# Kernel tuning notes

Hardware: AMD Instinct MI355X
Metric: run time of the kernel (lower is better)

The kernel has to match this reference:

```python
import jax, jax.numpy as jnp
import numpy as np

N = 16384      # points
C = 512        # channels (d_model)
D_INNER = 1024 # expand=2
D_STATE = 16
D_CONV = 4
DT_RANK = 32   # ceil(C/16)
MLP = 1024     # mlp_ratio=2
EPS = 1e-5


def setup_inputs() -> dict:
    key = jax.random.key(0)
    ks = jax.random.split(key, 16)
    s = 0.02
    feat = jax.random.normal(ks[0], (N, C), jnp.float32)
    perm = np.random.RandomState(0).permutation(N)
    order = jnp.asarray(perm, jnp.int32)
    inverse = jnp.asarray(np.argsort(perm), jnp.int32)
    inp = dict(
        feat=feat, order=order, inverse=inverse,
        ln1_w=jnp.ones((C,)), ln1_b=jnp.zeros((C,)),
        in_proj_w=s * jax.random.normal(ks[1], (2 * D_INNER, C)),
        conv_w=s * jax.random.normal(ks[2], (D_INNER, D_CONV)),
        conv_b=jnp.zeros((D_INNER,)),
        x_proj_w=s * jax.random.normal(ks[3], (DT_RANK + 2 * D_STATE, D_INNER)),
        dt_proj_w=s * jax.random.normal(ks[4], (D_INNER, DT_RANK)),
        dt_proj_b=jnp.full((D_INNER,), -2.0),  # softplus(-2) ~ small dt, like mamba init
        A_log=jnp.log(jnp.tile(jnp.arange(1, D_STATE + 1, dtype=jnp.float32)[None, :], (D_INNER, 1))),
        D_skip=jnp.ones((D_INNER,)),
        out_proj_w=s * jax.random.normal(ks[5], (C, D_INNER)),
        ln2_w=jnp.ones((C,)), ln2_b=jnp.zeros((C,)),
        ffn_w1=s * jax.random.normal(ks[6], (C, MLP)), ffn_b1=jnp.zeros((MLP,)),
        ffn_w2=s * jax.random.normal(ks[7], (MLP, C)), ffn_b2=jnp.zeros((C,)),
    )
    return inp


def _layer_norm(x, w, b):
    mu = jnp.mean(x, axis=-1, keepdims=True)
    var = jnp.mean(jnp.square(x - mu), axis=-1, keepdims=True)
    return (x - mu) * jax.lax.rsqrt(var + EPS) * w + b


def _mamba(x, in_proj_w, conv_w, conv_b, x_proj_w, dt_proj_w, dt_proj_b,
           A_log, D_skip, out_proj_w):
    # x: (L, C)
    L = x.shape[0]
    xz = x @ in_proj_w.T                      # (L, 2*D_INNER)
    xm, z = jnp.split(xz, 2, axis=-1)
    # depthwise causal conv1d, kernel D_CONV
    xp = jnp.pad(xm, ((D_CONV - 1, 0), (0, 0)))
    xc = conv_b + sum(xp[k:k + L] * conv_w[:, k] for k in range(D_CONV))
    xc = jax.nn.silu(xc)                      # (L, D_INNER)
    dbc = xc @ x_proj_w.T                     # (L, DT_RANK + 2*D_STATE)
    dt, Bm, Cm = jnp.split(dbc, [DT_RANK, DT_RANK + D_STATE], axis=-1)
    dt = jax.nn.softplus(dt @ dt_proj_w.T + dt_proj_b)  # (L, D_INNER)
    A = -jnp.exp(A_log)                       # (D_INNER, D_STATE)

    def step(h, inp):
        dt_t, B_t, C_t, x_t = inp             # (D_INNER,), (D_STATE,), (D_STATE,), (D_INNER,)
        dA = jnp.exp(dt_t[:, None] * A)       # (D_INNER, D_STATE)
        h = dA * h + (dt_t * x_t)[:, None] * B_t[None, :]
        return h, h @ C_t                     # y_t: (D_INNER,)

    h0 = jnp.zeros((D_INNER, D_STATE), xm.dtype)
    _, ys = jax.lax.scan(step, h0, (dt, Bm, Cm, xc))
    y = (ys + xc * D_skip) * jax.nn.silu(z)
    return y @ out_proj_w.T                   # (L, C)


def reference(feat, order, inverse, ln1_w, ln1_b, in_proj_w, conv_w, conv_b,
              x_proj_w, dt_proj_w, dt_proj_b, A_log, D_skip, out_proj_w,
              ln2_w, ln2_b, ffn_w1, ffn_b1, ffn_w2, ffn_b2):
    f = feat[order]                           # gather by serialized order
    x = f + _mamba(_layer_norm(f, ln1_w, ln1_b), in_proj_w, conv_w, conv_b,
                   x_proj_w, dt_proj_w, dt_proj_b, A_log, D_skip, out_proj_w)
    h = _layer_norm(x, ln2_w, ln2_b)
    x = x + (jax.nn.gelu(h @ ffn_w1 + ffn_b1, approximate=False) @ ffn_w2 + ffn_b2)
    return x[inverse]                         # scatter back to original order
```

## Files before the change

kernel.cpp:

```cpp
#include <hip/hip_runtime.h>


#define DEV __device__ __forceinline__

typedef unsigned short u16;
typedef u16    u16x8  __attribute__((ext_vector_type(8)));
typedef __bf16 bf16x8 __attribute__((ext_vector_type(8)));
typedef float  f32x4  __attribute__((ext_vector_type(4)));

static constexpr int L_SEQ = 16384;
static constexpr int LC    = 64;
static constexpr int NCH   = 256;

DEV u16 f2b(float x){
  union { float f; unsigned u; } c; c.f = x;
  unsigned u = c.u;
  return (u16)((u + 0x7fffu + ((u >> 16) & 1u)) >> 16);
}
DEV float b2f(u16 h){
  union { unsigned u; float f; } c; c.u = ((unsigned)h) << 16;
  return c.f;
}
DEV int ldix(const void* p, int l, bool is64){
  return is64 ? (int)((const long long*)p)[l] : ((const int*)p)[l];
}
DEV float siluf(float x){ return x / (1.f + __expf(-x)); }
DEV float softplusf(float x){ return x > 20.f ? x : log1pf(__expf(x)); }
DEV float geluf(float x){ return 0.5f * x * (1.f + erff(x * 0.70710678118f)); }

DEV void gld_lds16(const u16* g, u16* l){
  __builtin_amdgcn_global_load_lds(
      (const __attribute__((address_space(1))) unsigned*)g,
      (__attribute__((address_space(3))) unsigned*)l, 16, 0, 0);
}

DEV void pow16(float r, float* a){
  float r2 = r * r, r4 = r2 * r2, r8 = r4 * r4;
  a[0] = r;        a[1] = r2;       a[2] = r2 * r;    a[3] = r4;
  a[4] = r4 * r;   a[5] = r4 * r2;  a[6] = r4 * a[2]; a[7] = r8;
  a[8] = r8 * r;   a[9] = r8 * r2;  a[10] = r8 * a[2]; a[11] = r8 * r4;
  a[12] = r8 * a[4]; a[13] = r8 * a[5]; a[14] = r8 * a[6]; a[15] = r8 * r8;
}

__global__ __launch_bounds__(256) void fill_k(float* out, float v, unsigned n){
  unsigned i = blockIdx.x * 256 + threadIdx.x;
  if (i < n) out[i] = v;
}

__global__ void detect_k(const int* ord32, int* flag){
  flag[0] = (ord32[1] == 0 && ord32[3] == 0 && ord32[5] == 0) ? 1 : 0;
  flag[1] = 0;
}

__global__ __launch_bounds__(256) void checkA_k(const float* __restrict__ alog,
                                                int* flag){
  int i = blockIdx.x * 256 + threadIdx.x;
  int s = i & 15;
  float v = alog[i];
  float base = alog[i - s];
  if (fabsf(v - (base + __logf((float)(s + 1)))) > 1e-4f) atomicOr(flag + 1, 1);
}

struct NT4 { const float* src[4]; unsigned off[5]; };
__global__ __launch_bounds__(256) void normw_k(NT4 t, u16* dst){
  unsigned i = blockIdx.x * 256 + threadIdx.x;
  if (i >= t.off[4]) return;
  int s = 0;
  #pragma unroll
  for (int k = 1; k <= 3; k++) s += (i >= t.off[k]) ? 1 : 0;
  dst[i] = f2b(t.src[s][i - t.off[s]]);
}

__global__ __launch_bounds__(256) void convT_kernel(const float* __restrict__ in,
                                                    u16* __restrict__ out, int K, int N){
  __shared__ float t[32][33];
  int k0 = blockIdx.x * 32, n0 = blockIdx.y * 32;
  int tx = threadIdx.x & 31, ty = threadIdx.x >> 5;
  #pragma unroll
  for (int i = 0; i < 32; i += 8)
    t[ty + i][tx] = in[(size_t)(k0 + ty + i) * N + n0 + tx];
  __syncthreads();
  #pragma unroll
  for (int i = 0; i < 32; i += 8)
    out[(size_t)(n0 + ty + i) * K + k0 + tx] = f2b(t[tx][ty + i]);
}

__global__ __launch_bounds__(256) void gather_ln1(const float* __restrict__ feat,
    const void* order, const float* __restrict__ w, const float* __restrict__ b,
    const int* flag, u16* __restrict__ x1b){
  __shared__ float rs_[256], rq_[256];
  const bool is64 = flag[0] != 0;
  int l = blockIdx.x, tid = threadIdx.x;
  int src = ldix(order, l, is64);
  float v0 = feat[(size_t)src * 512 + tid];
  float v1 = feat[(size_t)src * 512 + tid + 256];
  rs_[tid] = v0 + v1; rq_[tid] = v0 * v0 + v1 * v1;
  __syncthreads();
  for (int o = 128; o; o >>= 1){
    if (tid < o){ rs_[tid] += rs_[tid + o]; rq_[tid] += rq_[tid + o]; }
    __syncthreads();
  }
  float mu = rs_[0] * (1.f / 512.f);
  float var = rq_[0] * (1.f / 512.f) - mu * mu;
  float rstd = rsqrtf(var + 1e-5f);
  x1b[(size_t)l * 512 + tid]       = f2b((v0 - mu) * rstd * w[tid]       + b[tid]);
  x1b[(size_t)l * 512 + tid + 256] = f2b((v1 - mu) * rstd * w[tid + 256] + b[tid + 256]);
}

__global__ __launch_bounds__(256) void ln2_kernel(const float* __restrict__ x,
    const float* __restrict__ w, const float* __restrict__ b, u16* __restrict__ h2b){
  __shared__ float rs_[256], rq_[256];
  int l = blockIdx.x, tid = threadIdx.x;
  float v0 = x[(size_t)l * 512 + tid];
  float v1 = x[(size_t)l * 512 + tid + 256];
  rs_[tid] = v0 + v1; rq_[tid] = v0 * v0 + v1 * v1;
  __syncthreads();
  for (int o = 128; o; o >>= 1){
    if (tid < o){ rs_[tid] += rs_[tid + o]; rq_[tid] += rq_[tid + o]; }
    __syncthreads();
  }
  float mu = rs_[0] * (1.f / 512.f);
  float var = rq_[0] * (1.f / 512.f) - mu * mu;
  float rstd = rsqrtf(var + 1e-5f);
  h2b[(size_t)l * 512 + tid]       = f2b((v0 - mu) * rstd * w[tid]       + b[tid]);
  h2b[(size_t)l * 512 + tid + 256] = f2b((v1 - mu) * rstd * w[tid + 256] + b[tid + 256]);
}

__global__ __launch_bounds__(256) void conv_silu(const u16* __restrict__ xm,
    const float* __restrict__ cw, const float* __restrict__ cb, u16* __restrict__ xcb){
  constexpr int TT = 8;
  const int tid = threadIdx.x;
  const int d0 = (tid & 127) * 8;
  const int t0 = (blockIdx.x * 2 + (tid >> 7)) * TT;

  float wk[4][8], bias[8];
  #pragma unroll
  for (int j = 0; j < 8; j++) bias[j] = cb[d0 + j];
  #pragma unroll
  for (int j = 0; j < 8; j++){
    f32x4 v = *(const f32x4*)(cw + (d0 + j) * 4);
    wk[0][j] = v[0]; wk[1][j] = v[1]; wk[2][j] = v[2]; wk[3][j] = v[3];
  }

  float win[3][8];
  #pragma unroll
  for (int k = 0; k < 3; k++){
    int tt = t0 - 3 + k;
    if (tt >= 0){
      u16x8 v = *(const u16x8*)(xm + (size_t)tt * 1024 + d0);
      #pragma unroll
      for (int j = 0; j < 8; j++) win[k][j] = b2f(v[j]);
    } else {
      #pragma unroll
      for (int j = 0; j < 8; j++) win[k][j] = 0.f;
    }
  }

  #pragma unroll
  for (int t = 0; t < TT; t++){
    u16x8 v = *(const u16x8*)(xm + (size_t)(t0 + t) * 1024 + d0);
    u16x8 o;
    float cu[8];
    #pragma unroll
    for (int j = 0; j < 8; j++){
      cu[j] = b2f(v[j]);
      float acc = bias[j] + win[0][j] * wk[0][j] + win[1][j] * wk[1][j]
                + win[2][j] * wk[2][j] + cu[j] * wk[3][j];
      o[j] = f2b(siluf(acc));
    }
    *(u16x8*)(xcb + (size_t)(t0 + t) * 1024 + d0) = o;
    #pragma unroll
    for (int j = 0; j < 8; j++){
      win[0][j] = win[1][j]; win[1][j] = win[2][j]; win[2][j] = cu[j];
    }
  }
}

enum { M_BF16 = 0, M_INPROJ = 1, M_DT = 2, M_RES = 3, M_GELU = 4, M_FFN2 = 5 };

template<int BM, int BN, int WM, int WN, int MODE>
__global__ __launch_bounds__(256) void gemm_bt(
    const u16* __restrict__ A, const u16* __restrict__ B,
    int N, int K, int lda, int ldb,
    float* __restrict__ outf, u16* __restrict__ outb, u16* __restrict__ outb2,
    const float* __restrict__ auxf, const float* __restrict__ auxw,
    const void* ordv, const int* flag){
  constexpr int BK = 32;
  constexpr int MI = WM / 16, NI = WN / 16;
  constexpr int WCOLS = BN / WN;
  constexpr int NA = BM * 4 / 256;
  constexpr int NB = BN * 4 / 256;
  __shared__ __align__(16) u16 sA[BM * BK];
  __shared__ __align__(16) u16 sB[BN * BK];
  const int tid  = threadIdx.x;
  const int wave = tid >> 6, lane = tid & 63;
  const int wr = wave / WCOLS, wc = wave % WCOLS;
  const int m0 = blockIdx.x * BM, n0 = blockIdx.y * BN;
  const int rr = lane & 15;
  const int qk = (lane >> 4) * 8;

  f32x4 acc[MI][NI] = {};

  for (int k0 = 0; k0 < K; k0 += BK){
    #pragma unroll
    for (int i = 0; i < NA; i++){
      int idx = tid + i * 256;
      int r = idx >> 2, c = (idx & 3) * 8;
      gld_lds16(A + (size_t)(m0 + r) * lda + k0 + c, sA + (size_t)idx * 8);
    }
    #pragma unroll
    for (int i = 0; i < NB; i++){
      int idx = tid + i * 256;
      int r = idx >> 2, c = (idx & 3) * 8;
      gld_lds16(B + (size_t)(n0 + r) * ldb + k0 + c, sB + (size_t)idx * 8);
    }
    __syncthreads();

    bf16x8 af[MI], bfr[NI];
    #pragma unroll
    for (int i = 0; i < MI; i++)
      af[i] = *(const bf16x8*)(sA + (wr * WM + i * 16 + rr) * BK + qk);
    #pragma unroll
    for (int j = 0; j < NI; j++)
      bfr[j] = *(const bf16x8*)(sB + (wc * WN + j * 16 + rr) * BK + qk);
    #pragma unroll
    for (int i = 0; i < MI; i++)
      #pragma unroll
      for (int j = 0; j < NI; j++)
        acc[i][j] = __builtin_amdgcn_mfma_f32_16x16x32_bf16(af[i], bfr[j], acc[i][j], 0, 0, 0);
    __syncthreads();
  }

  const bool is64 = flag ? (flag[0] != 0) : false;
  #pragma unroll
  for (int i = 0; i < MI; i++){
    #pragma unroll
    for (int j = 0; j < NI; j++){
      #pragma unroll
      for (int r = 0; r < 4; r++){
        int m = m0 + wr * WM + i * 16 + ((lane >> 4) << 2) + r;
        int n = n0 + wc * WN + j * 16 + (lane & 15);
        float v = acc[i][j][r];
        size_t o = (size_t)m * N + n;
        if constexpr (MODE == M_BF16){
          outb[o] = f2b(v);
        } else if constexpr (MODE == M_INPROJ){
          if (n < 1024) outb [(size_t)m * 1024 + n]          = f2b(v);
          else          outb2[(size_t)m * 1024 + (n - 1024)] = f2b(siluf(v));
        } else if constexpr (MODE == M_DT){
          outb[o] = f2b(softplusf(v + auxw[n]));
        } else if constexpr (MODE == M_RES){
          int src = ldix(ordv, m, is64);
          outf[o] = v + auxw[(size_t)src * 512 + n];
        } else if constexpr (MODE == M_GELU){
          outb[o] = f2b(geluf(v + auxw[n]));
        } else {
          outf[o] = v + auxw[n] + auxf[o];
        }
      }
    }
  }
}

__global__ __launch_bounds__(256) void scan_pass1(const u16* __restrict__ dt,
    const u16* __restrict__ xc, const u16* __restrict__ dbc,
    const float* __restrict__ alog, const int* __restrict__ flag,
    u16* __restrict__ chP, u16* __restrict__ chH){
  __shared__ float sB[LC * 16];
  const int chunk = blockIdx.x;
  const int d = blockIdx.y * 256 + threadIdx.x;
  const int t0 = chunk * LC;
  for (int i = threadIdx.x; i < LC * 16; i += 256){
    int t = i >> 4, s = i & 15;
    sB[i] = b2f(dbc[(size_t)(t0 + t) * 64 + 32 + s]);
  }
  __syncthreads();
  float h[16];
  #pragma unroll
  for (int s = 0; s < 16; s++) h[s] = 0.f;
  float P[16];
  const bool fastA = (flag[1] == 0);
  if (fastA){
    const float a0 = -__expf(alog[(size_t)d * 16]);
    float R = 1.f;
    for (int t = 0; t < LC; t++){
      float dtv = b2f(dt[(size_t)(t0 + t) * 1024 + d]);
      float xv  = b2f(xc[(size_t)(t0 + t) * 1024 + d]);
      float dtx = dtv * xv;
      float r = __expf(dtv * a0);
      R *= r;
      float a_[16];
      pow16(r, a_);
      #pragma unroll
      for (int s = 0; s < 16; s++)
        h[s] = a_[s] * h[s] + dtx * sB[t * 16 + s];
    }
    pow16(R, P);
  } else {
    float A[16];
    #pragma unroll
    for (int s = 0; s < 16; s++){
      A[s] = -__expf(alog[(size_t)d * 16 + s]);
      P[s] = 1.f;
    }
    for (int t = 0; t < LC; t++){
      float dtv = b2f(dt[(size_t)(t0 + t) * 1024 + d]);
      float xv  = b2f(xc[(size_t)(t0 + t) * 1024 + d]);
      float dtx = dtv * xv;
      #pragma unroll
      for (int s = 0; s < 16; s++){
        float a = __expf(dtv * A[s]);
        P[s] *= a;
        h[s] = a * h[s] + dtx * sB[t * 16 + s];
      }
    }
  }
  #pragma unroll
  for (int s = 0; s < 16; s++){
    chP[((size_t)chunk * 16 + s) * 1024 + d] = f2b(P[s]);
    chH[((size_t)chunk * 16 + s) * 1024 + d] = f2b(h[s]);
  }
}

__global__ __launch_bounds__(64) void carry_scan(const u16* chP, const u16* chH,
                                                 u16* hin){
  int id = blockIdx.x * 64 + threadIdx.x;
  float h = 0.f;
  for (int k = 0; k < NCH; k += 8){
    float P[8], E[8];
    #pragma unroll
    for (int j = 0; j < 8; j++){
      P[j] = b2f(chP[(size_t)(k + j) * 16384 + id]);
      E[j] = b2f(chH[(size_t)(k + j) * 16384 + id]);
    }
    #pragma unroll
    for (int j = 0; j < 8; j++){
      hin[(size_t)(k + j) * 16384 + id] = f2b(h);
      h = P[j] * h + E[j];
    }
  }
}

__global__ __launch_bounds__(256) void scan_pass3(const u16* __restrict__ dt,
    const u16* xc, const u16* __restrict__ dbc,
    const float* __restrict__ alog, const int* __restrict__ flag,
    const u16* __restrict__ hin,
    const float* __restrict__ dskip, const u16* __restrict__ zsil, u16* yb){
  __shared__ float sBC[LC * 32];
  const int chunk = blockIdx.x;
  const int d = blockIdx.y * 256 + threadIdx.x;
  const int t0 = chunk * LC;
  for (int i = threadIdx.x; i < LC * 32; i += 256){
    int t = i >> 5, c = i & 31;
    sBC[i] = b2f(dbc[(size_t)(t0 + t) * 64 + 32 + c]);
  }
  __syncthreads();
  float h[16];
  #pragma unroll
  for (int s = 0; s < 16; s++)
    h[s] = b2f(hin[((size_t)chunk * 16 + s) * 1024 + d]);
  const float Dv = dskip[d];
  const bool fastA = (flag[1] == 0);
  if (fastA){
    const float a0 = -__expf(alog[(size_t)d * 16]);
    for (int t = 0; t < LC; t++){
      float dtv = b2f(dt[(size_t)(t0 + t) * 1024 + d]);
      float xv  = b2f(xc[(size_t)(t0 + t) * 1024 + d]);
      float dtx = dtv * xv;
      float r = __expf(dtv * a0);
      float a_[16];
      pow16(r, a_);
      float y = 0.f;
      #pragma unroll
      for (int s = 0; s < 16; s++){
        h[s] = a_[s] * h[s] + dtx * sBC[t * 32 + s];
        y += h[s] * sBC[t * 32 + 16 + s];
      }
      float rv = (y + xv * Dv) * b2f(zsil[(size_t)(t0 + t) * 1024 + d]);
      yb[(size_t)(t0 + t) * 1024 + d] = f2b(rv);
    }
  } else {
    float A[16];
    #pragma unroll
    for (int s = 0; s < 16; s++) A[s] = -__expf(alog[(size_t)d * 16 + s]);
    for (int t = 0; t < LC; t++){
      float dtv = b2f(dt[(size_t)(t0 + t) * 1024 + d]);
      float xv  = b2f(xc[(size_t)(t0 + t) * 1024 + d]);
      float dtx = dtv * xv;
      float y = 0.f;
      #pragma unroll
      for (int s = 0; s < 16; s++){
        float a = __expf(dtv * A[s]);
        h[s] = a * h[s] + dtx * sBC[t * 32 + s];
        y += h[s] * sBC[t * 32 + 16 + s];
      }
      float rv = (y + xv * Dv) * b2f(zsil[(size_t)(t0 + t) * 1024 + d]);
      yb[(size_t)(t0 + t) * 1024 + d] = f2b(rv);
    }
  }
}

__global__ __launch_bounds__(256) void final_gather(const float* __restrict__ xfin,
    const void* inv, const int* flag, float* __restrict__ out){
  const bool is64 = flag[0] != 0;
  int i = blockIdx.x, tid = threadIdx.x;
  int src = ldix(inv, i, is64);
  out[(size_t)i * 512 + tid]       = xfin[(size_t)src * 512 + tid];
  out[(size_t)i * 512 + tid + 256] = xfin[(size_t)src * 512 + tid + 256];
}

extern "C" void kernel_launch(void* const* d_in, const int* in_sizes, int n_in,
                              void* d_out, int out_size, void* d_ws, size_t ws_size,
                              hipStream_t stream){
  float* out = (float*)d_out;
  char* w = (char*)d_ws;

  constexpr size_t OFF_W1T  = 3342336;
  constexpr size_t OFF_W2T  = OFF_W1T + 1048576;
  constexpr size_t OFF_FLAG = OFF_W2T + 1048576;
  constexpr size_t OFF_XMB  = 5439744;
  constexpr size_t OFF_ZSIL = OFF_XMB  + 33554432;
  constexpr size_t OFF_XCB  = OFF_ZSIL + 33554432;
  constexpr size_t OFF_X1B  = OFF_XCB  + 33554432;
  constexpr size_t OFF_DBC  = OFF_X1B  + 16777216;
  constexpr size_t OFF_CHP  = OFF_X1B;
  constexpr size_t OFF_CHH  = OFF_X1B  + 8388608;
  constexpr size_t WS_NEED  = OFF_DBC  + 2097152;

  int code = 0;
  static const int want[20] = {8388608,16384,16384,512,512,1048576,4096,1024,
                               65536,32768,1024,16384,1024,524288,512,512,
                               524288,1024,524288,512};
  if (n_in != 20) code = 1000;
  else {
    for (int i = 0; i < 20 && !code; i++)
      if (in_sizes[i] != want[i]) code = 2000 + i * 50;
    if (!code && out_size != 8388608) code = 3000;
    if (!code && ws_size < WS_NEED)   code = 4000;
  }
  if (code){
    unsigned n = (unsigned)(out_size > 0 ? out_size : 1);
    fill_k<<<(n + 255) / 256, 256, 0, stream>>>(out, (float)code, n);
    return;
  }

  u16*   w1tb = (u16*)(w + OFF_W1T);
  u16*   w2tb = (u16*)(w + OFF_W2T);
  int*   flag = (int*)(w + OFF_FLAG);
  u16*   xmb  = (u16*)(w + OFF_XMB);
  u16*   zsil = (u16*)(w + OFF_ZSIL);
  u16*   xcb  = (u16*)(w + OFF_XCB);
  u16*   x1b  = (u16*)(w + OFF_X1B);
  u16*   dbcb = (u16*)(w + OFF_DBC);
  u16*   chP  = (u16*)(w + OFF_CHP);
  u16*   chH  = (u16*)(w + OFF_CHH);
  float* x    = (float*)(w + OFF_XMB);
  float* xfin = (float*)(w + OFF_XCB);
  u16* dtb  = xmb;
  u16* yb   = xcb;
  u16* midb = zsil;
  u16* h2b  = x1b;
  u16* hin  = chP;

  u16* nb = (u16*)w;
  u16* inpjn  = nb;
  u16* xpjn   = nb + 1048576;
  u16* dtpjn  = nb + 1114112;
  u16* outpjn = nb + 1146880;
  NT4 t;
  t.src[0] = (const float*)d_in[5];  t.src[1] = (const float*)d_in[8];
  t.src[2] = (const float*)d_in[9];  t.src[3] = (const float*)d_in[13];
  t.off[0] = 0; t.off[1] = 1048576; t.off[2] = 1114112; t.off[3] = 1146880; t.off[4] = 1671168;

  detect_k<<<1, 1, 0, stream>>>((const int*)d_in[1], flag);
  checkA_k<<<64, 256, 0, stream>>>((const float*)d_in[11], flag);
  normw_k<<<(1671168 + 255) / 256, 256, 0, stream>>>(t, nb);
  convT_kernel<<<dim3(16, 32), 256, 0, stream>>>((const float*)d_in[16], w1tb, 512, 1024);
  convT_kernel<<<dim3(32, 16), 256, 0, stream>>>((const float*)d_in[18], w2tb, 1024, 512);

  gather_ln1<<<L_SEQ, 256, 0, stream>>>((const float*)d_in[0], d_in[1],
      (const float*)d_in[3], (const float*)d_in[4], flag, x1b);

  gemm_bt<128,128,64,64,M_INPROJ><<<dim3(128,16),256,0,stream>>>(
      x1b, inpjn, 2048, 512, 512, 512, nullptr, xmb, zsil, nullptr, nullptr, nullptr, nullptr);

  conv_silu<<<1024, 256, 0, stream>>>(xmb,
      (const float*)d_in[6], (const float*)d_in[7], xcb);

  gemm_bt<64,64,16,64,M_BF16><<<dim3(256,1),256,0,stream>>>(
      xcb, xpjn, 64, 1024, 1024, 1024, nullptr, dbcb, nullptr, nullptr, nullptr, nullptr, nullptr);

  gemm_bt<128,128,64,64,M_DT><<<dim3(128,8),256,0,stream>>>(
      dbcb, dtpjn, 1024, 32, 64, 32, nullptr, dtb, nullptr, nullptr,
      (const float*)d_in[10], nullptr, nullptr);

  scan_pass1<<<dim3(NCH,4),256,0,stream>>>(dtb, xcb, dbcb,
      (const float*)d_in[11], flag, chP, chH);
  carry_scan<<<256,64,0,stream>>>(chP, chH, hin);
  scan_pass3<<<dim3(NCH,4),256,0,stream>>>(dtb, xcb, dbcb,
      (const float*)d_in[11], flag, hin, (const float*)d_in[12], zsil, yb);

  gemm_bt<128,128,64,64,M_RES><<<dim3(128,4),256,0,stream>>>(
      yb, outpjn, 512, 1024, 1024, 1024, x, nullptr, nullptr, nullptr,
      (const float*)d_in[0], d_in[1], flag);

  ln2_kernel<<<L_SEQ,256,0,stream>>>(x, (const float*)d_in[14], (const float*)d_in[15], h2b);

  gemm_bt<128,128,64,64,M_GELU><<<dim3(128,8),256,0,stream>>>(
      h2b, w1tb, 1024, 512, 512, 512, nullptr, midb, nullptr, nullptr,
      (const float*)d_in[17], nullptr, nullptr);

  gemm_bt<128,128,64,64,M_FFN2><<<dim3(128,4),256,0,stream>>>(
      midb, w2tb, 512, 1024, 1024, 1024, xfin, nullptr, nullptr, x,
      (const float*)d_in[19], nullptr, nullptr);

  final_gather<<<L_SEQ,256,0,stream>>>(xfin, d_in[2], flag, out);
}
```

Before: 562.4 us.

## Add double-buffered BK=64 GEMM with swizzled LDS and use it for main projections

Adds a new GEMM kernel that uses a 64-wide K step, two LDS buffers so the next tile's global-to-LDS load overlaps the current tile's MFMAs, and an XOR swizzle on LDS column groups to avoid bank conflicts. The in_proj, x_proj, out_proj and both FFN GEMMs switch to it, and the epilogue is moved into a shared helper. LDS use doubles per block, which may lower occupancy, in exchange for fewer barriers and better latency hiding.

Result: faster. 528.1 us (-6.1%).

```diff
diff --git a/kernel.cpp b/kernel.cpp
--- a/kernel.cpp
+++ b/kernel.cpp
@@ -177,6 +177,112 @@
 }
 
 enum { M_BF16 = 0, M_INPROJ = 1, M_DT = 2, M_RES = 3, M_GELU = 4, M_FFN2 = 5 };
+
+template<int MODE>
+DEV void gemm_epilogue(float v, int m, int n, int N,
+    float* __restrict__ outf, u16* __restrict__ outb, u16* __restrict__ outb2,
+    const float* __restrict__ auxf, const float* __restrict__ auxw,
+    const void* ordv, bool is64){
+  size_t o = (size_t)m * N + n;
+  if constexpr (MODE == M_BF16){
+    outb[o] = f2b(v);
+  } else if constexpr (MODE == M_INPROJ){
+    if (n < 1024) outb [(size_t)m * 1024 + n]          = f2b(v);
+    else          outb2[(size_t)m * 1024 + (n - 1024)] = f2b(siluf(v));
+  } else if constexpr (MODE == M_DT){
+    outb[o] = f2b(softplusf(v + auxw[n]));
+  } else if constexpr (MODE == M_RES){
+    int src = ldix(ordv, m, is64);
+    outf[o] = v + auxw[(size_t)src * 512 + n];
+  } else if constexpr (MODE == M_GELU){
+    outb[o] = f2b(geluf(v + auxw[n]));
+  } else {
+    outf[o] = v + auxw[n] + auxf[o];
+  }
+}
+
+template<int BM, int BN, int WM, int WN, int MODE>
+__global__ __launch_bounds__(256) void gemm_bt64(
+    const u16* __restrict__ A, const u16* __restrict__ B,
+    int N, int K, int lda, int ldb,
+    float* __restrict__ outf, u16* __restrict__ outb, u16* __restrict__ outb2,
+    const float* __restrict__ auxf, const float* __restrict__ auxw,
+    const void* ordv, const int* flag){
+  constexpr int BK = 64;
+  constexpr int MI = WM / 16, NI = WN / 16;
+  constexpr int WCOLS = BN / WN;
+  constexpr int NA = BM * BK / (256 * 8);
+  constexpr int NB = BN * BK / (256 * 8);
+  __shared__ __align__(16) u16 sA[2][BM * BK];
+  __shared__ __align__(16) u16 sB[2][BN * BK];
+  const int tid  = threadIdx.x;
+  const int wave = tid >> 6, lane = tid & 63;
+  const int wr = wave / WCOLS, wc = wave % WCOLS;
+  const int m0 = blockIdx.x * BM, n0 = blockIdx.y * BN;
+  const int rr = lane & 15;
+  const int qh = lane >> 4;
+
+  f32x4 acc[MI][NI] = {};
+
+  auto stage = [&](int buf, int k0){
+    #pragma unroll
+    for (int i = 0; i < NA; i++){
+      int idx = tid + i * 256;
+      int row = idx >> 3, sub = idx & 7;
+      int cg = sub ^ (row & 7);
+      gld_lds16(A + (size_t)(m0 + row) * lda + k0 + cg * 8, &sA[buf][idx * 8]);
+    }
+    #pragma unroll
+    for (int i = 0; i < NB; i++){
+      int idx = tid + i * 256;
+      int row = idx >> 3, sub = idx & 7;
+      int cg = sub ^ (row & 7);
+      gld_lds16(B + (size_t)(n0 + row) * ldb + k0 + cg * 8, &sB[buf][idx * 8]);
+    }
+  };
+
+  stage(0, 0);
+  const int nst = K / BK;
+  for (int st = 0; st < nst; st++){
+    const int cur = st & 1;
+    __syncthreads();
+    if (st + 1 < nst) stage(cur ^ 1, (st + 1) * BK);
+    #pragma unroll
+    for (int kk = 0; kk < 2; kk++){
+      bf16x8 af[MI], bfr[NI];
+      #pragma unroll
+      for (int i = 0; i < MI; i++){
+        int R = wr * WM + i * 16 + rr;
+        int sub = (kk * 4 + qh) ^ (R & 7);
+        af[i] = *(const bf16x8*)(&sA[cur][R * BK + sub * 8]);
+      }
+      #pragma unroll
+      for (int j = 0; j < NI; j++){
+        int R = wc * WN + j * 16 + rr;
+        int sub = (kk * 4 + qh) ^ (R & 7);
+        bfr[j] = *(const bf16x8*)(&sB[cur][R * BK + sub * 8]);
+      }
+      #pragma unroll
+      for (int i = 0; i < MI; i++)
+        #pragma unroll
+        for (int j = 0; j < NI; j++)
+          acc[i][j] = __builtin_amdgcn_mfma_f32_16x16x32_bf16(af[i], bfr[j], acc[i][j], 0, 0, 0);
+    }
+  }
+
+  const bool is64 = flag ? (flag[0] != 0) : false;
+  #pragma unroll
+  for (int i = 0; i < MI; i++)
+    #pragma unroll
+    for (int j = 0; j < NI; j++)
+      #pragma unroll
+      for (int r = 0; r < 4; r++){
+        int m = m0 + wr * WM + i * 16 + ((lane >> 4) << 2) + r;
+        int n = n0 + wc * WN + j * 16 + (lane & 15);
+        gemm_epilogue<MODE>(acc[i][j][r], m, n, N, outf, outb, outb2,
+                            auxf, auxw, ordv, is64);
+      }
+}
 
 template<int BM, int BN, int WM, int WN, int MODE>
 __global__ __launch_bounds__(256) void gemm_bt(
@@ -233,33 +339,16 @@
 
   const bool is64 = flag ? (flag[0] != 0) : false;
   #pragma unroll
-  for (int i = 0; i < MI; i++){
-    #pragma unroll
-    for (int j = 0; j < NI; j++){
+  for (int i = 0; i < MI; i++)
+    #pragma unroll
+    for (int j = 0; j < NI; j++)
       #pragma unroll
       for (int r = 0; r < 4; r++){
         int m = m0 + wr * WM + i * 16 + ((lane >> 4) << 2) + r;
         int n = n0 + wc * WN + j * 16 + (lane & 15);
-        float v = acc[i][j][r];
-        size_t o = (size_t)m * N + n;
-        if constexpr (MODE == M_BF16){
-          outb[o] = f2b(v);
-        } else if constexpr (MODE == M_INPROJ){
-          if (n < 1024) outb [(size_t)m * 1024 + n]          = f2b(v);
-          else          outb2[(size_t)m * 1024 + (n - 1024)] = f2b(siluf(v));
-        } else if constexpr (MODE == M_DT){
-          outb[o] = f2b(softplusf(v + auxw[n]));
-        } else if constexpr (MODE == M_RES){
-          int src = ldix(ordv, m, is64);
-          outf[o] = v + auxw[(size_t)src * 512 + n];
-        } else if constexpr (MODE == M_GELU){
-          outb[o] = f2b(geluf(v + auxw[n]));
-        } else {
-          outf[o] = v + auxw[n] + auxf[o];
-        }
+        gemm_epilogue<MODE>(acc[i][j][r], m, n, N, outf, outb, outb2,
+                            auxf, auxw, ordv, is64);
       }
-    }
-  }
 }
 
 __global__ __launch_bounds__(256) void scan_pass1(const u16* __restrict__ dt,
@@ -481,13 +570,13 @@
   gather_ln1<<<L_SEQ, 256, 0, stream>>>((const float*)d_in[0], d_in[1],
       (const float*)d_in[3], (const float*)d_in[4], flag, x1b);
 
-  gemm_bt<128,128,64,64,M_INPROJ><<<dim3(128,16),256,0,stream>>>(
+  gemm_bt64<128,128,64,64,M_INPROJ><<<dim3(128,16),256,0,stream>>>(
       x1b, inpjn, 2048, 512, 512, 512, nullptr, xmb, zsil, nullptr, nullptr, nullptr, nullptr);
 
   conv_silu<<<1024, 256, 0, stream>>>(xmb,
       (const float*)d_in[6], (const float*)d_in[7], xcb);
 
-  gemm_bt<64,64,16,64,M_BF16><<<dim3(256,1),256,0,stream>>>(
+  gemm_bt64<64,64,16,64,M_BF16><<<dim3(256,1),256,0,stream>>>(
       xcb, xpjn, 64, 1024, 1024, 1024, nullptr, dbcb, nullptr, nullptr, nullptr, nullptr, nullptr);
 
   gemm_bt<128,128,64,64,M_DT><<<dim3(128,8),256,0,stream>>>(
@@ -500,17 +589,17 @@
   scan_pass3<<<dim3(NCH,4),256,0,stream>>>(dtb, xcb, dbcb,
       (const float*)d_in[11], flag, hin, (const float*)d_in[12], zsil, yb);
 
-  gemm_bt<128,128,64,64,M_RES><<<dim3(128,4),256,0,stream>>>(
+  gemm_bt64<128,128,64,64,M_RES><<<dim3(128,4),256,0,stream>>>(
       yb, outpjn, 512, 1024, 1024, 1024, x, nullptr, nullptr, nullptr,
       (const float*)d_in[0], d_in[1], flag);
 
   ln2_kernel<<<L_SEQ,256,0,stream>>>(x, (const float*)d_in[14], (const float*)d_in[15], h2b);
 
-  gemm_bt<128,128,64,64,M_GELU><<<dim3(128,8),256,0,stream>>>(
+  gemm_bt64<128,128,64,64,M_GELU><<<dim3(128,8),256,0,stream>>>(
       h2b, w1tb, 1024, 512, 512, 512, nullptr, midb, nullptr, nullptr,
       (const float*)d_in[17], nullptr, nullptr);
 
-  gemm_bt<128,128,64,64,M_FFN2><<<dim3(128,4),256,0,stream>>>(
+  gemm_bt64<128,128,64,64,M_FFN2><<<dim3(128,4),256,0,stream>>>(
       midb, w2tb, 512, 1024, 1024, 1024, xfin, nullptr, nullptr, x,
       (const float*)d_in[19], nullptr, nullptr);
 
```
